# Optimization experiments

Hardware: AMD Instinct MI355X
Metric: run time of the kernel (lower is better)

The kernel has to match this reference:

```python
import jax, jax.numpy as jnp
import numpy as np

FEAT_STRIDE = 16
SCORE_THRESH = 0.7
MAX_OUTPUTS = 50


def setup_inputs() -> dict:
    key = jax.random.key(0)
    k1, k2 = jax.random.split(key)
    B = 4096
    img_width = 16384
    feat_width = img_width // FEAT_STRIDE  # 1024
    pred_cls_logit = jax.random.normal(k1, (B, feat_width), dtype=jnp.float32)
    pred_delta = jax.random.normal(k2, (B, feat_width, 2), dtype=jnp.float32)
    return {"pred_cls_logit": pred_cls_logit, "pred_delta": pred_delta, "img_width": img_width}


def _nms_single(positions, scores):
    # positions: [N,2] float32, scores: [N] float32 (post-sigmoid)
    # TF version gathers entries with score >= thresh; we keep fixed shape with a
    # validity mask (score of invalid entries set to -inf) for jit-compatibility.
    valid = scores >= SCORE_THRESH
    cent = positions.mean(axis=1)                       # [N]
    n = jnp.sum(valid).astype(jnp.float32)
    vmin = jnp.min(jnp.where(valid, cent, jnp.inf))
    vmax = jnp.max(jnp.where(valid, cent, -jnp.inf))
    # note: the original code OVERWRITES the distance_thresh arg with this value
    dthresh = 0.55 * (vmax - vmin) / (n - 1.0)
    neg_inf = jnp.float32(-jnp.inf)
    work = jnp.where(valid, scores, neg_inf)

    def step(work, _):
        idx = jnp.argmax(work)                          # greedy: highest remaining score
        ok = work[idx] > neg_inf                        # any candidate left?
        sel_s = scores[idx]
        sel_p = positions[idx]
        sel_c = cent[idx]
        # TF keeps |dist| > thresh, i.e. suppress |dist| <= thresh (incl. self)
        suppress = jnp.abs(cent - sel_c) <= dthresh
        work = jnp.where(suppress, neg_inf, work)
        out_p = jnp.where(ok, sel_p, 0.0)               # pad_to_fixed_size -> zeros
        out_s = jnp.where(ok, sel_s, 0.0)
        return work, (out_p, out_s)

    _, (nms_pos, nms_sc) = jax.lax.scan(step, work, None, length=MAX_OUTPUTS)
    return nms_pos, nms_sc[:, None]                     # [50,2], [50,1]


def reference(pred_cls_logit, pred_delta, img_width):
    feat_width = pred_delta.shape[1]
    # interval centers, broadcast over the 2-wide position pair
    centers = (jnp.arange(feat_width, dtype=jnp.float32) + 0.5) * FEAT_STRIDE  # [Fw]
    pos = pred_delta * FEAT_STRIDE + centers[None, :, None]                    # [B,Fw,2]
    w = jnp.float32(img_width)
    pos = jnp.clip(pos, 0.0, w - 1.0)
    scores = jax.nn.sigmoid(pred_cls_logit)                                    # [B,Fw]
    nms_positions, nms_scores = jax.vmap(_nms_single)(pos, scores)
    return nms_positions, nms_scores
```

## Files before the change

kernel.cpp:

```cpp
#include <hip/hip_runtime.h>
#include <stdint.h>

typedef unsigned int u32;

#define FW   1024
#define NOUT 50
#define RPB  4
#define CAP  320
#define SPL  5

#define DPP_UMAX_STEP(m, ctrl)                                                 \
  do {                                                                         \
    const u32 _t = (u32)__builtin_amdgcn_update_dpp(0, (int)(m), (ctrl),       \
                                                    0xf, 0xf, false);          \
    (m) = (m) > _t ? (m) : _t;                                                 \
  } while (0)
#define DPP_FMAX_STEP(m, ctrl)                                                 \
  do {                                                                         \
    const float _t = __uint_as_float((u32)__builtin_amdgcn_update_dpp(         \
        __float_as_int(m), __float_as_int(m), (ctrl), 0xf, 0xf, false));       \
    (m) = fmaxf((m), _t);                                                      \
  } while (0)
#define DPP_FMIN_STEP(m, ctrl)                                                 \
  do {                                                                         \
    const float _t = __uint_as_float((u32)__builtin_amdgcn_update_dpp(         \
        __float_as_int(m), __float_as_int(m), (ctrl), 0xf, 0xf, false));       \
    (m) = fminf((m), _t);                                                      \
  } while (0)
#define DPP_SCAN_STEP(x, ctrl, rmask)                                          \
  do {                                                                         \
    const int _t = __builtin_amdgcn_update_dpp(0, (x), (ctrl), (rmask), 0xf,   \
                                               false);                         \
    (x) += _t;                                                                 \
  } while (0)

#define DPP_ALL6(OP, a)                                                        \
  OP(a, 0x111); OP(a, 0x112); OP(a, 0x114); OP(a, 0x118); OP(a, 0x142);        \
  OP(a, 0x143)

__device__ __forceinline__ u32 umax2(u32 a, u32 b) { return a > b ? a : b; }
__device__ __forceinline__ u32 umax3(u32 a, u32 b, u32 c) {
  return umax2(umax2(a, b), c);
}

template <int NS>
__device__ __forceinline__ u32 run_nms(const float2* __restrict__ kc, int nc,
                                       int lane, float dthresh) {
  u32 keys[NS];
  float cents[NS];
  {
    float2 sl[NS];
#pragma unroll
    for (int k = 0; k < NS; ++k) sl[k] = kc[k * 64 + lane];
#pragma unroll
    for (int k = 0; k < NS; ++k) {
      const int q2 = k * 64 + lane;
      keys[k]  = (q2 < nc) ? __float_as_uint(sl[k].x) : 0u;
      cents[k] = sl[k].y;
    }
  }

  u32 acckey = 0;
#pragma unroll
  for (int it = 0; it < NOUT; ++it) {
    u32 m = umax3(keys[0], keys[1], keys[2]);
#pragma unroll
    for (int k = 3; k < NS; ++k) m = umax2(m, keys[k]);
    DPP_UMAX_STEP(m, 0x111);
    DPP_UMAX_STEP(m, 0x112);
    DPP_UMAX_STEP(m, 0x114);
    DPP_UMAX_STEP(m, 0x118);
    DPP_UMAX_STEP(m, 0x142);
    DPP_UMAX_STEP(m, 0x143);
    const u32 best = (u32)__builtin_amdgcn_readlane((int)m, 63);

    const int qs  = 511 - (int)(best & 511u);
    const int qsc = qs < CAP ? qs : CAP - 1;
    const float sel_c = kc[qsc].y;

    acckey = (lane == it) ? best : acckey;

#pragma unroll
    for (int k = 0; k < NS; ++k) {
      keys[k] = (fabsf(cents[k] - sel_c) <= dthresh) ? 0u : keys[k];
    }
  }
  return acckey;
}

__global__ __launch_bounds__(256, 4) void nms1d_kernel(
    const float* __restrict__ logits,
    const float* __restrict__ delta,
    const int* __restrict__ iw_p,
    float* __restrict__ out_pos,
    float* __restrict__ out_sc)
{
  const int wave = threadIdx.x >> 6;
  const int lane = threadIdx.x & 63;
  const int b = blockIdx.x * RPB + wave;

  __shared__ float2 s_kc[RPB][CAP + 1];
  __shared__ float2 s_pp[RPB][CAP + 1];
  float2* __restrict__ kc = s_kc[wave];
  float2* __restrict__ pp = s_pp[wave];

  const float hi = (float)(*iw_p) - 1.0f;

  const float* __restrict__ lrow = logits + (size_t)b * FW;
  const float* __restrict__ drow = delta  + (size_t)b * FW * 2;

  float4 xl0 = *(const float4*)(lrow + lane * 16 + 0);
  float4 xl1 = *(const float4*)(lrow + lane * 16 + 4);
  float4 xl2 = *(const float4*)(lrow + lane * 16 + 8);
  float4 xl3 = *(const float4*)(lrow + lane * 16 + 12);
  float4 dA0 = *(const float4*)(drow + lane * 32 + 0);
  float4 dB0 = *(const float4*)(drow + lane * 32 + 4);
  float4 dA1 = *(const float4*)(drow + lane * 32 + 8);
  float4 dB1 = *(const float4*)(drow + lane * 32 + 12);
  float4 dA2 = *(const float4*)(drow + lane * 32 + 16);
  float4 dB2 = *(const float4*)(drow + lane * 32 + 20);
  float4 dA3 = *(const float4*)(drow + lane * 32 + 24);
  float4 dB3 = *(const float4*)(drow + lane * 32 + 28);

  float sc[16];
  int v = 0;
  const float4 xls[4] = {xl0, xl1, xl2, xl3};
#pragma unroll
  for (int c = 0; c < 4; ++c) {
    const float xs[4] = {xls[c].x, xls[c].y, xls[c].z, xls[c].w};
#pragma unroll
    for (int j = 0; j < 4; ++j) {
      const float s = 1.0f / (1.0f + expf(-xs[j]));
      sc[c * 4 + j] = s;
      v += (s >= 0.7f) ? 1 : 0;
    }
  }

  int incl = v;
  DPP_SCAN_STEP(incl, 0x111, 0xf);
  DPP_SCAN_STEP(incl, 0x112, 0xf);
  DPP_SCAN_STEP(incl, 0x114, 0xf);
  DPP_SCAN_STEP(incl, 0x118, 0xf);
  DPP_SCAN_STEP(incl, 0x142, 0xa);
  DPP_SCAN_STEP(incl, 0x143, 0xc);
  const int base = incl - v;
  const int n = __builtin_amdgcn_readlane(incl, 63);

  float vmin = INFINITY, vmax = -INFINITY;
  int q = base;
  const float4 dAs[4] = {dA0, dA1, dA2, dA3};
  const float4 dBs[4] = {dB0, dB1, dB2, dB3};
#pragma unroll
  for (int c = 0; c < 4; ++c) {
    const float dx[4] = {dAs[c].x, dAs[c].z, dBs[c].x, dBs[c].z};
    const float dy[4] = {dAs[c].y, dAs[c].w, dBs[c].y, dBs[c].w};
#pragma unroll
    for (int j = 0; j < 4; ++j) {
      const int e = c * 4 + j;
      const int f = lane * 16 + e;
      const float center = (float)f * 16.0f + 8.0f;
      float p0 = dx[j] * 16.0f + center;
      float p1 = dy[j] * 16.0f + center;
      p0 = fminf(fmaxf(p0, 0.0f), hi);
      p1 = fminf(fmaxf(p1, 0.0f), hi);
      const float cc = (p0 + p1) * 0.5f;
      const float s = sc[e];
      const bool valid = (s >= 0.7f);
      vmin = valid ? fminf(vmin, cc) : vmin;
      vmax = valid ? fmaxf(vmax, cc) : vmax;
      const int qd = (valid && q < CAP) ? q : CAP;
      const u32 key = ((__float_as_uint(s) - 0x3F333333u) << 9) | (u32)(511 - q);
      kc[qd] = make_float2(__uint_as_float(key), cc);
      pp[qd] = make_float2(p0, p1);
      q += valid ? 1 : 0;
    }
  }

  DPP_ALL6(DPP_FMIN_STEP, vmin);
  DPP_ALL6(DPP_FMAX_STEP, vmax);
  const float dt_part = (0.55f * (vmax - vmin)) / ((float)incl - 1.0f);
  const float dthresh = __uint_as_float(
      (u32)__builtin_amdgcn_readlane(__float_as_int(dt_part), 63));

  const int nc = n < CAP ? n : CAP;
  u32 acckey;
  if (nc <= 256) acckey = run_nms<4>(kc, nc, lane, dthresh);
  else           acckey = run_nms<5>(kc, nc, lane, dthresh);

  if (lane < NOUT) {
    float p0 = 0.0f, p1 = 0.0f, s = 0.0f;
    if (acckey != 0u) {
      const int qw = 511 - (int)(acckey & 511u);
      const float2 sl = pp[qw];
      p0 = sl.x;
      p1 = sl.y;
      s  = __uint_as_float((acckey >> 9) + 0x3F333333u);
    }
    float* __restrict__ orow_p = out_pos + (size_t)b * NOUT * 2;
    float* __restrict__ orow_s = out_sc  + (size_t)b * NOUT;
    *(float2*)(orow_p + lane * 2) = make_float2(p0, p1);
    orow_s[lane] = s;
  }
}

extern "C" void kernel_launch(void* const* d_in, const int* in_sizes, int n_in,
                              void* d_out, int out_size, void* d_ws, size_t ws_size,
                              hipStream_t stream) {
  const float* logits = (const float*)d_in[0];
  const float* delta  = (const float*)d_in[1];
  const int*   iw     = (const int*)d_in[2];
  const int B = in_sizes[0] / FW;
  float* out_pos = (float*)d_out;
  float* out_sc  = (float*)d_out + (size_t)B * NOUT * 2;
  nms1d_kernel<<<(B + RPB - 1) / RPB, RPB * 64, 0, stream>>>(logits, delta, iw, out_pos, out_sc);
}
```

Measured before the change: 25.69 us.

## Process two rows per wave with interleaved NMS loops for ILP

Each wave now handles two batch rows and runs their greedy NMS loops interleaved, so the serial max-reduce, readlane and LDS-lookup chains of one row can overlap with the other's. This aims to hide the latency of the dependent per-iteration reduction. In exchange register pressure roughly doubles (launch bounds drop from 4 to 2 blocks per SM), there are half as many waves in total, and the 5-slot path runs whenever either row needs it.

```diff
diff --git a/kernel.cpp b/kernel.cpp
--- a/kernel.cpp
+++ b/kernel.cpp
@@ -5,7 +5,8 @@
 
 #define FW   1024
 #define NOUT 50
-#define RPB  4
+#define WPB  4
+#define RPW  2
 #define CAP  320
 #define SPL  5
 
@@ -44,51 +45,67 @@
 }
 
 template <int NS>
-__device__ __forceinline__ u32 run_nms(const float2* __restrict__ kc, int nc,
-                                       int lane, float dthresh) {
-  u32 keys[NS];
-  float cents[NS];
+__device__ __forceinline__ void run_nms2(
+    const float2* __restrict__ kcA, const float2* __restrict__ kcB,
+    int ncA, int ncB, int lane, float dtA, float dtB,
+    u32& accA_o, u32& accB_o)
+{
+  u32 keysA[NS], keysB[NS];
+  float centsA[NS], centsB[NS];
   {
-    float2 sl[NS];
-#pragma unroll
-    for (int k = 0; k < NS; ++k) sl[k] = kc[k * 64 + lane];
+    float2 slA[NS], slB[NS];
+#pragma unroll
+    for (int k = 0; k < NS; ++k) {
+      slA[k] = kcA[k * 64 + lane];
+      slB[k] = kcB[k * 64 + lane];
+    }
 #pragma unroll
     for (int k = 0; k < NS; ++k) {
       const int q2 = k * 64 + lane;
-      keys[k]  = (q2 < nc) ? __float_as_uint(sl[k].x) : 0u;
-      cents[k] = sl[k].y;
-    }
-  }
-
-  u32 acckey = 0;
-#pragma unroll
+      keysA[k]  = (q2 < ncA) ? __float_as_uint(slA[k].x) : 0u;
+      keysB[k]  = (q2 < ncB) ? __float_as_uint(slB[k].x) : 0u;
+      centsA[k] = slA[k].y;
+      centsB[k] = slB[k].y;
+    }
+  }
+
+  u32 accA = 0, accB = 0;
+#pragma unroll 2
   for (int it = 0; it < NOUT; ++it) {
-    u32 m = umax3(keys[0], keys[1], keys[2]);
-#pragma unroll
-    for (int k = 3; k < NS; ++k) m = umax2(m, keys[k]);
-    DPP_UMAX_STEP(m, 0x111);
-    DPP_UMAX_STEP(m, 0x112);
-    DPP_UMAX_STEP(m, 0x114);
-    DPP_UMAX_STEP(m, 0x118);
-    DPP_UMAX_STEP(m, 0x142);
-    DPP_UMAX_STEP(m, 0x143);
-    const u32 best = (u32)__builtin_amdgcn_readlane((int)m, 63);
-
-    const int qs  = 511 - (int)(best & 511u);
-    const int qsc = qs < CAP ? qs : CAP - 1;
-    const float sel_c = kc[qsc].y;
-
-    acckey = (lane == it) ? best : acckey;
+    u32 mA = umax3(keysA[0], keysA[1], keysA[2]);
+    u32 mB = umax3(keysB[0], keysB[1], keysB[2]);
+#pragma unroll
+    for (int k = 3; k < NS; ++k) { mA = umax2(mA, keysA[k]); mB = umax2(mB, keysB[k]); }
+    DPP_UMAX_STEP(mA, 0x111); DPP_UMAX_STEP(mB, 0x111);
+    DPP_UMAX_STEP(mA, 0x112); DPP_UMAX_STEP(mB, 0x112);
+    DPP_UMAX_STEP(mA, 0x114); DPP_UMAX_STEP(mB, 0x114);
+    DPP_UMAX_STEP(mA, 0x118); DPP_UMAX_STEP(mB, 0x118);
+    DPP_UMAX_STEP(mA, 0x142); DPP_UMAX_STEP(mB, 0x142);
+    DPP_UMAX_STEP(mA, 0x143); DPP_UMAX_STEP(mB, 0x143);
+    const u32 bestA = (u32)__builtin_amdgcn_readlane((int)mA, 63);
+    const u32 bestB = (u32)__builtin_amdgcn_readlane((int)mB, 63);
+
+    const int qsA  = 511 - (int)(bestA & 511u);
+    const int qsB  = 511 - (int)(bestB & 511u);
+    const int qscA = qsA < CAP ? qsA : CAP - 1;
+    const int qscB = qsB < CAP ? qsB : CAP - 1;
+    const float selA = kcA[qscA].y;
+    const float selB = kcB[qscB].y;
+
+    accA = (lane == it) ? bestA : accA;
+    accB = (lane == it) ? bestB : accB;
 
 #pragma unroll
     for (int k = 0; k < NS; ++k) {
-      keys[k] = (fabsf(cents[k] - sel_c) <= dthresh) ? 0u : keys[k];
-    }
-  }
-  return acckey;
-}
-
-__global__ __launch_bounds__(256, 4) void nms1d_kernel(
+      keysA[k] = (fabsf(centsA[k] - selA) <= dtA) ? 0u : keysA[k];
+      keysB[k] = (fabsf(centsB[k] - selB) <= dtB) ? 0u : keysB[k];
+    }
+  }
+  accA_o = accA;
+  accB_o = accB;
+}
+
+__global__ __launch_bounds__(256, 2) void nms1d_kernel(
     const float* __restrict__ logits,
     const float* __restrict__ delta,
     const int* __restrict__ iw_p,
@@ -97,109 +114,126 @@
 {
   const int wave = threadIdx.x >> 6;
   const int lane = threadIdx.x & 63;
-  const int b = blockIdx.x * RPB + wave;
-
-  __shared__ float2 s_kc[RPB][CAP + 1];
-  __shared__ float2 s_pp[RPB][CAP + 1];
-  float2* __restrict__ kc = s_kc[wave];
-  float2* __restrict__ pp = s_pp[wave];
+  const int b0 = (blockIdx.x * WPB + wave) * RPW;
+
+  __shared__ float2 s_kc[WPB][RPW][CAP + 1];
+  __shared__ float2 s_pp[WPB][RPW][CAP + 1];
 
   const float hi = (float)(*iw_p) - 1.0f;
 
-  const float* __restrict__ lrow = logits + (size_t)b * FW;
-  const float* __restrict__ drow = delta  + (size_t)b * FW * 2;
-
-  float4 xl0 = *(const float4*)(lrow + lane * 16 + 0);
-  float4 xl1 = *(const float4*)(lrow + lane * 16 + 4);
-  float4 xl2 = *(const float4*)(lrow + lane * 16 + 8);
-  float4 xl3 = *(const float4*)(lrow + lane * 16 + 12);
-  float4 dA0 = *(const float4*)(drow + lane * 32 + 0);
-  float4 dB0 = *(const float4*)(drow + lane * 32 + 4);
-  float4 dA1 = *(const float4*)(drow + lane * 32 + 8);
-  float4 dB1 = *(const float4*)(drow + lane * 32 + 12);
-  float4 dA2 = *(const float4*)(drow + lane * 32 + 16);
-  float4 dB2 = *(const float4*)(drow + lane * 32 + 20);
-  float4 dA3 = *(const float4*)(drow + lane * 32 + 24);
-  float4 dB3 = *(const float4*)(drow + lane * 32 + 28);
-
-  float sc[16];
-  int v = 0;
-  const float4 xls[4] = {xl0, xl1, xl2, xl3};
-#pragma unroll
-  for (int c = 0; c < 4; ++c) {
-    const float xs[4] = {xls[c].x, xls[c].y, xls[c].z, xls[c].w};
-#pragma unroll
-    for (int j = 0; j < 4; ++j) {
-      const float s = 1.0f / (1.0f + expf(-xs[j]));
-      sc[c * 4 + j] = s;
-      v += (s >= 0.7f) ? 1 : 0;
-    }
-  }
-
-  int incl = v;
-  DPP_SCAN_STEP(incl, 0x111, 0xf);
-  DPP_SCAN_STEP(incl, 0x112, 0xf);
-  DPP_SCAN_STEP(incl, 0x114, 0xf);
-  DPP_SCAN_STEP(incl, 0x118, 0xf);
-  DPP_SCAN_STEP(incl, 0x142, 0xa);
-  DPP_SCAN_STEP(incl, 0x143, 0xc);
-  const int base = incl - v;
-  const int n = __builtin_amdgcn_readlane(incl, 63);
-
-  float vmin = INFINITY, vmax = -INFINITY;
-  int q = base;
-  const float4 dAs[4] = {dA0, dA1, dA2, dA3};
-  const float4 dBs[4] = {dB0, dB1, dB2, dB3};
-#pragma unroll
-  for (int c = 0; c < 4; ++c) {
-    const float dx[4] = {dAs[c].x, dAs[c].z, dBs[c].x, dBs[c].z};
-    const float dy[4] = {dAs[c].y, dAs[c].w, dBs[c].y, dBs[c].w};
-#pragma unroll
-    for (int j = 0; j < 4; ++j) {
-      const int e = c * 4 + j;
-      const int f = lane * 16 + e;
-      const float center = (float)f * 16.0f + 8.0f;
-      float p0 = dx[j] * 16.0f + center;
-      float p1 = dy[j] * 16.0f + center;
-      p0 = fminf(fmaxf(p0, 0.0f), hi);
-      p1 = fminf(fmaxf(p1, 0.0f), hi);
-      const float cc = (p0 + p1) * 0.5f;
-      const float s = sc[e];
-      const bool valid = (s >= 0.7f);
-      vmin = valid ? fminf(vmin, cc) : vmin;
-      vmax = valid ? fmaxf(vmax, cc) : vmax;
-      const int qd = (valid && q < CAP) ? q : CAP;
-      const u32 key = ((__float_as_uint(s) - 0x3F333333u) << 9) | (u32)(511 - q);
-      kc[qd] = make_float2(__uint_as_float(key), cc);
-      pp[qd] = make_float2(p0, p1);
-      q += valid ? 1 : 0;
-    }
-  }
-
-  DPP_ALL6(DPP_FMIN_STEP, vmin);
-  DPP_ALL6(DPP_FMAX_STEP, vmax);
-  const float dt_part = (0.55f * (vmax - vmin)) / ((float)incl - 1.0f);
-  const float dthresh = __uint_as_float(
-      (u32)__builtin_amdgcn_readlane(__float_as_int(dt_part), 63));
-
-  const int nc = n < CAP ? n : CAP;
-  u32 acckey;
-  if (nc <= 256) acckey = run_nms<4>(kc, nc, lane, dthresh);
-  else           acckey = run_nms<5>(kc, nc, lane, dthresh);
+  float4 xl[RPW][4], dXa[RPW][4], dXb[RPW][4];
+#pragma unroll
+  for (int r = 0; r < RPW; ++r) {
+    const float* __restrict__ lrow = logits + (size_t)(b0 + r) * FW;
+#pragma unroll
+    for (int c = 0; c < 4; ++c)
+      xl[r][c] = *(const float4*)(lrow + lane * 16 + 4 * c);
+  }
+#pragma unroll
+  for (int r = 0; r < RPW; ++r) {
+    const float* __restrict__ drow = delta + (size_t)(b0 + r) * FW * 2;
+#pragma unroll
+    for (int c = 0; c < 4; ++c) {
+      dXa[r][c] = *(const float4*)(drow + lane * 32 + 8 * c);
+      dXb[r][c] = *(const float4*)(drow + lane * 32 + 8 * c + 4);
+    }
+  }
+
+  float sc[RPW][16];
+  int incl[RPW], base_[RPW];
+#pragma unroll
+  for (int r = 0; r < RPW; ++r) {
+    int v = 0;
+#pragma unroll
+    for (int c = 0; c < 4; ++c) {
+      const float xs[4] = {xl[r][c].x, xl[r][c].y, xl[r][c].z, xl[r][c].w};
+#pragma unroll
+      for (int j = 0; j < 4; ++j) {
+        const float s = 1.0f / (1.0f + expf(-xs[j]));
+        sc[r][c * 4 + j] = s;
+        v += (s >= 0.7f) ? 1 : 0;
+      }
+    }
+    int ic = v;
+    DPP_SCAN_STEP(ic, 0x111, 0xf);
+    DPP_SCAN_STEP(ic, 0x112, 0xf);
+    DPP_SCAN_STEP(ic, 0x114, 0xf);
+    DPP_SCAN_STEP(ic, 0x118, 0xf);
+    DPP_SCAN_STEP(ic, 0x142, 0xa);
+    DPP_SCAN_STEP(ic, 0x143, 0xc);
+    incl[r]  = ic;
+    base_[r] = ic - v;
+  }
+
+  float dthr[RPW];
+  int nfin[RPW];
+#pragma unroll
+  for (int r = 0; r < RPW; ++r) {
+    float2* __restrict__ kc = s_kc[wave][r];
+    float2* __restrict__ pp = s_pp[wave][r];
+    float vmin = INFINITY, vmax = -INFINITY;
+    int q = base_[r];
+#pragma unroll
+    for (int c = 0; c < 4; ++c) {
+      const float dx[4] = {dXa[r][c].x, dXa[r][c].z, dXb[r][c].x, dXb[r][c].z};
+      const float dy[4] = {dXa[r][c].y, dXa[r][c].w, dXb[r][c].y, dXb[r][c].w};
+#pragma unroll
+      for (int j = 0; j < 4; ++j) {
+        const int e = c * 4 + j;
+        const int f = lane * 16 + e;
+        const float center = (float)f * 16.0f + 8.0f;
+        float p0 = dx[j] * 16.0f + center;
+        float p1 = dy[j] * 16.0f + center;
+        p0 = fminf(fmaxf(p0, 0.0f), hi);
+        p1 = fminf(fmaxf(p1, 0.0f), hi);
+        const float cc = (p0 + p1) * 0.5f;
+        const float s = sc[r][e];
+        const bool valid = (s >= 0.7f);
+        vmin = valid ? fminf(vmin, cc) : vmin;
+        vmax = valid ? fmaxf(vmax, cc) : vmax;
+        const int qd = (valid && q < CAP) ? q : CAP;
+        const u32 key = ((__float_as_uint(s) - 0x3F333333u) << 9) | (u32)(511 - q);
+        kc[qd] = make_float2(__uint_as_float(key), cc);
+        pp[qd] = make_float2(p0, p1);
+        q += valid ? 1 : 0;
+      }
+    }
+    DPP_ALL6(DPP_FMIN_STEP, vmin);
+    DPP_ALL6(DPP_FMAX_STEP, vmax);
+    const float dt_part = (0.55f * (vmax - vmin)) / ((float)incl[r] - 1.0f);
+    dthr[r] = __uint_as_float(
+        (u32)__builtin_amdgcn_readlane(__float_as_int(dt_part), 63));
+    nfin[r] = __builtin_amdgcn_readlane(incl[r], 63);
+  }
+
+  const int ncA = nfin[0] < CAP ? nfin[0] : CAP;
+  const int ncB = nfin[1] < CAP ? nfin[1] : CAP;
+  u32 accA, accB;
+  if (ncA <= 256 && ncB <= 256)
+    run_nms2<4>(s_kc[wave][0], s_kc[wave][1], ncA, ncB, lane,
+                dthr[0], dthr[1], accA, accB);
+  else
+    run_nms2<5>(s_kc[wave][0], s_kc[wave][1], ncA, ncB, lane,
+                dthr[0], dthr[1], accA, accB);
 
   if (lane < NOUT) {
-    float p0 = 0.0f, p1 = 0.0f, s = 0.0f;
-    if (acckey != 0u) {
-      const int qw = 511 - (int)(acckey & 511u);
-      const float2 sl = pp[qw];
-      p0 = sl.x;
-      p1 = sl.y;
-      s  = __uint_as_float((acckey >> 9) + 0x3F333333u);
-    }
-    float* __restrict__ orow_p = out_pos + (size_t)b * NOUT * 2;
-    float* __restrict__ orow_s = out_sc  + (size_t)b * NOUT;
-    *(float2*)(orow_p + lane * 2) = make_float2(p0, p1);
-    orow_s[lane] = s;
+#pragma unroll
+    for (int r = 0; r < RPW; ++r) {
+      const u32 ak = (r == 0) ? accA : accB;
+      const float2* __restrict__ pp = s_pp[wave][r];
+      float p0 = 0.0f, p1 = 0.0f, s = 0.0f;
+      if (ak != 0u) {
+        const int qw = 511 - (int)(ak & 511u);
+        const float2 sl = pp[qw];
+        p0 = sl.x;
+        p1 = sl.y;
+        s  = __uint_as_float((ak >> 9) + 0x3F333333u);
+      }
+      float* __restrict__ orow_p = out_pos + (size_t)(b0 + r) * NOUT * 2;
+      float* __restrict__ orow_s = out_sc  + (size_t)(b0 + r) * NOUT;
+      *(float2*)(orow_p + lane * 2) = make_float2(p0, p1);
+      orow_s[lane] = s;
+    }
   }
 }
 
@@ -212,5 +246,7 @@
   const int B = in_sizes[0] / FW;
   float* out_pos = (float*)d_out;
   float* out_sc  = (float*)d_out + (size_t)B * NOUT * 2;
-  nms1d_kernel<<<(B + RPB - 1) / RPB, RPB * 64, 0, stream>>>(logits, delta, iw, out_pos, out_sc);
-}
+  const int rows_per_block = WPB * RPW;
+  nms1d_kernel<<<(B + rows_per_block - 1) / rows_per_block, WPB * 64, 0, stream>>>(
+      logits, delta, iw, out_pos, out_sc);
+}
```

Result: slower. 27.28 us (+6.2%).

## Select top-two candidates per NMS iteration to halve serial greedy steps

Applied to the files above, without the earlier changes.

Each NMS iteration now runs a wave-wide top-2 reduction (max and second max via DPP) instead of only the max. If the runner-up is not suppressed by the winner, both are accepted in one pass, so the serial loop of 50 argmax rounds can take fewer rounds. The cost is a roughly doubled reduction and suppression per iteration, plus a loop that is no longer fully unrolled and runs a data-dependent number of times. The second-max tracking in the DPP step must be exactly right for results to stay correct.

```diff
diff --git a/kernel.cpp b/kernel.cpp
--- a/kernel.cpp
+++ b/kernel.cpp
@@ -15,6 +15,16 @@
                                                     0xf, 0xf, false);          \
     (m) = (m) > _t ? (m) : _t;                                                 \
   } while (0)
+#define DPP_UMAX2_STEP(m1, m2, ctrl)                                           \
+  do {                                                                         \
+    const u32 _t1 = (u32)__builtin_amdgcn_update_dpp(0, (int)(m1), (ctrl),     \
+                                                     0xf, 0xf, false);         \
+    const u32 _t2 = (u32)__builtin_amdgcn_update_dpp(0, (int)(m2), (ctrl),     \
+                                                     0xf, 0xf, false);         \
+    const u32 _c = (m1) < _t1 ? (m1) : _t1;              \
+    (m1) = (m1) > _t1 ? (m1) : _t1;                                            \
+    (m2) = umax3((m2), _t2, _c);                                               \
+  } while (0)
 #define DPP_FMAX_STEP(m, ctrl)                                                 \
   do {                                                                         \
     const float _t = __uint_as_float((u32)__builtin_amdgcn_update_dpp(         \
@@ -39,6 +49,7 @@
   OP(a, 0x143)
 
 __device__ __forceinline__ u32 umax2(u32 a, u32 b) { return a > b ? a : b; }
+__device__ __forceinline__ u32 umin2(u32 a, u32 b) { return a < b ? a : b; }
 __device__ __forceinline__ u32 umax3(u32 a, u32 b, u32 c) {
   return umax2(umax2(a, b), c);
 }
@@ -60,30 +71,47 @@
     }
   }
 
+  const float dnan = __uint_as_float(0x7FC00000u);
   u32 acckey = 0;
-#pragma unroll
-  for (int it = 0; it < NOUT; ++it) {
-    u32 m = umax3(keys[0], keys[1], keys[2]);
-#pragma unroll
-    for (int k = 3; k < NS; ++k) m = umax2(m, keys[k]);
-    DPP_UMAX_STEP(m, 0x111);
-    DPP_UMAX_STEP(m, 0x112);
-    DPP_UMAX_STEP(m, 0x114);
-    DPP_UMAX_STEP(m, 0x118);
-    DPP_UMAX_STEP(m, 0x142);
-    DPP_UMAX_STEP(m, 0x143);
-    const u32 best = (u32)__builtin_amdgcn_readlane((int)m, 63);
-
-    const int qs  = 511 - (int)(best & 511u);
-    const int qsc = qs < CAP ? qs : CAP - 1;
-    const float sel_c = kc[qsc].y;
-
-    acckey = (lane == it) ? best : acckey;
+  int it = 0;
+  while (it < NOUT) {
+    u32 m1 = umax2(keys[0], keys[1]);
+    u32 m2 = umin2(keys[0], keys[1]);
+#pragma unroll
+    for (int k = 2; k < NS; ++k) {
+      const u32 t = umin2(m1, keys[k]);
+      m1 = umax2(m1, keys[k]);
+      m2 = umax2(m2, t);
+    }
+    DPP_UMAX2_STEP(m1, m2, 0x111);
+    DPP_UMAX2_STEP(m1, m2, 0x112);
+    DPP_UMAX2_STEP(m1, m2, 0x114);
+    DPP_UMAX2_STEP(m1, m2, 0x118);
+    DPP_UMAX2_STEP(m1, m2, 0x142);
+    DPP_UMAX2_STEP(m1, m2, 0x143);
+    const u32 best1 = (u32)__builtin_amdgcn_readlane((int)m1, 63);
+    const u32 best2 = (u32)__builtin_amdgcn_readlane((int)m2, 63);
+
+    const int qs1  = 511 - (int)(best1 & 511u);
+    const int qs2  = 511 - (int)(best2 & 511u);
+    const int qsc1 = qs1 < CAP ? qs1 : CAP - 1;
+    const int qsc2 = qs2 < CAP ? qs2 : CAP - 1;
+    const float c1 = kc[qsc1].y;
+    const float c2 = kc[qsc2].y;
+
+    const bool acc2 = fabsf(c2 - c1) > dthresh;
+    const float dt2 = acc2 ? dthresh : dnan;
+
+    acckey = (lane == it) ? best1 : acckey;
+    acckey = (acc2 && lane == it + 1) ? best2 : acckey;
 
 #pragma unroll
     for (int k = 0; k < NS; ++k) {
-      keys[k] = (fabsf(cents[k] - sel_c) <= dthresh) ? 0u : keys[k];
-    }
+      keys[k] = (fabsf(cents[k] - c1) <= dthresh) ? 0u : keys[k];
+      keys[k] = (fabsf(cents[k] - c2) <= dt2)     ? 0u : keys[k];
+    }
+
+    it += __builtin_amdgcn_readfirstlane(acc2 ? 2 : 1);
   }
   return acckey;
 }
```

Result: slower. 27.95 us (+8.8%).

## Process two rows per wave, prefetching second row during first row's NMS

Applied to the files above, without the earlier changes.

Each wave now handles two batch rows. The global loads for the second row are issued before the first row's greedy NMS loop, so memory latency overlaps with compute. The grid is halved and launch bounds drop to 2 blocks per CU, which allows more registers for the prefetched data but may reduce occupancy and latency hiding across waves. There is also a risk that the compiler serializes the second row's loads or that the prefetched row spills registers.

```diff
diff --git a/kernel.cpp b/kernel.cpp
--- a/kernel.cpp
+++ b/kernel.cpp
@@ -5,7 +5,8 @@
 
 #define FW   1024
 #define NOUT 50
-#define RPB  4
+#define WPB  4
+#define RPW  2
 #define CAP  320
 #define SPL  5
 
@@ -43,91 +44,35 @@
   return umax2(umax2(a, b), c);
 }
 
-template <int NS>
-__device__ __forceinline__ u32 run_nms(const float2* __restrict__ kc, int nc,
-                                       int lane, float dthresh) {
-  u32 keys[NS];
-  float cents[NS];
-  {
-    float2 sl[NS];
-#pragma unroll
-    for (int k = 0; k < NS; ++k) sl[k] = kc[k * 64 + lane];
-#pragma unroll
-    for (int k = 0; k < NS; ++k) {
-      const int q2 = k * 64 + lane;
-      keys[k]  = (q2 < nc) ? __float_as_uint(sl[k].x) : 0u;
-      cents[k] = sl[k].y;
-    }
-  }
-
-  u32 acckey = 0;
-#pragma unroll
-  for (int it = 0; it < NOUT; ++it) {
-    u32 m = umax3(keys[0], keys[1], keys[2]);
-#pragma unroll
-    for (int k = 3; k < NS; ++k) m = umax2(m, keys[k]);
-    DPP_UMAX_STEP(m, 0x111);
-    DPP_UMAX_STEP(m, 0x112);
-    DPP_UMAX_STEP(m, 0x114);
-    DPP_UMAX_STEP(m, 0x118);
-    DPP_UMAX_STEP(m, 0x142);
-    DPP_UMAX_STEP(m, 0x143);
-    const u32 best = (u32)__builtin_amdgcn_readlane((int)m, 63);
-
-    const int qs  = 511 - (int)(best & 511u);
-    const int qsc = qs < CAP ? qs : CAP - 1;
-    const float sel_c = kc[qsc].y;
-
-    acckey = (lane == it) ? best : acckey;
-
-#pragma unroll
-    for (int k = 0; k < NS; ++k) {
-      keys[k] = (fabsf(cents[k] - sel_c) <= dthresh) ? 0u : keys[k];
-    }
-  }
-  return acckey;
-}
-
-__global__ __launch_bounds__(256, 4) void nms1d_kernel(
-    const float* __restrict__ logits,
-    const float* __restrict__ delta,
-    const int* __restrict__ iw_p,
-    float* __restrict__ out_pos,
-    float* __restrict__ out_sc)
-{
-  const int wave = threadIdx.x >> 6;
-  const int lane = threadIdx.x & 63;
-  const int b = blockIdx.x * RPB + wave;
-
-  __shared__ float2 s_kc[RPB][CAP + 1];
-  __shared__ float2 s_pp[RPB][CAP + 1];
-  float2* __restrict__ kc = s_kc[wave];
-  float2* __restrict__ pp = s_pp[wave];
-
-  const float hi = (float)(*iw_p) - 1.0f;
-
+struct RowData {
+  float4 xl[4];
+  float4 da[4];
+  float4 db[4];
+};
+
+__device__ __forceinline__ void load_row(const float* __restrict__ logits,
+                                         const float* __restrict__ delta,
+                                         int b, int lane, RowData& d) {
   const float* __restrict__ lrow = logits + (size_t)b * FW;
   const float* __restrict__ drow = delta  + (size_t)b * FW * 2;
-
-  float4 xl0 = *(const float4*)(lrow + lane * 16 + 0);
-  float4 xl1 = *(const float4*)(lrow + lane * 16 + 4);
-  float4 xl2 = *(const float4*)(lrow + lane * 16 + 8);
-  float4 xl3 = *(const float4*)(lrow + lane * 16 + 12);
-  float4 dA0 = *(const float4*)(drow + lane * 32 + 0);
-  float4 dB0 = *(const float4*)(drow + lane * 32 + 4);
-  float4 dA1 = *(const float4*)(drow + lane * 32 + 8);
-  float4 dB1 = *(const float4*)(drow + lane * 32 + 12);
-  float4 dA2 = *(const float4*)(drow + lane * 32 + 16);
-  float4 dB2 = *(const float4*)(drow + lane * 32 + 20);
-  float4 dA3 = *(const float4*)(drow + lane * 32 + 24);
-  float4 dB3 = *(const float4*)(drow + lane * 32 + 28);
-
+#pragma unroll
+  for (int c = 0; c < 4; ++c)
+    d.xl[c] = *(const float4*)(lrow + lane * 16 + 4 * c);
+#pragma unroll
+  for (int c = 0; c < 4; ++c) {
+    d.da[c] = *(const float4*)(drow + lane * 32 + 8 * c);
+    d.db[c] = *(const float4*)(drow + lane * 32 + 8 * c + 4);
+  }
+}
+
+__device__ __forceinline__ void prep_row(const RowData& d, float2* __restrict__ kc,
+                                         float2* __restrict__ pp, int lane,
+                                         float hi, float& dthresh_o, int& nc_o) {
   float sc[16];
   int v = 0;
-  const float4 xls[4] = {xl0, xl1, xl2, xl3};
 #pragma unroll
   for (int c = 0; c < 4; ++c) {
-    const float xs[4] = {xls[c].x, xls[c].y, xls[c].z, xls[c].w};
+    const float xs[4] = {d.xl[c].x, d.xl[c].y, d.xl[c].z, d.xl[c].w};
 #pragma unroll
     for (int j = 0; j < 4; ++j) {
       const float s = 1.0f / (1.0f + expf(-xs[j]));
@@ -148,12 +93,10 @@
 
   float vmin = INFINITY, vmax = -INFINITY;
   int q = base;
-  const float4 dAs[4] = {dA0, dA1, dA2, dA3};
-  const float4 dBs[4] = {dB0, dB1, dB2, dB3};
 #pragma unroll
   for (int c = 0; c < 4; ++c) {
-    const float dx[4] = {dAs[c].x, dAs[c].z, dBs[c].x, dBs[c].z};
-    const float dy[4] = {dAs[c].y, dAs[c].w, dBs[c].y, dBs[c].w};
+    const float dx[4] = {d.da[c].x, d.da[c].z, d.db[c].x, d.db[c].z};
+    const float dy[4] = {d.da[c].y, d.da[c].w, d.db[c].y, d.db[c].w};
 #pragma unroll
     for (int j = 0; j < 4; ++j) {
       const int e = c * 4 + j;
@@ -179,14 +122,60 @@
   DPP_ALL6(DPP_FMIN_STEP, vmin);
   DPP_ALL6(DPP_FMAX_STEP, vmax);
   const float dt_part = (0.55f * (vmax - vmin)) / ((float)incl - 1.0f);
-  const float dthresh = __uint_as_float(
+  dthresh_o = __uint_as_float(
       (u32)__builtin_amdgcn_readlane(__float_as_int(dt_part), 63));
-
-  const int nc = n < CAP ? n : CAP;
-  u32 acckey;
-  if (nc <= 256) acckey = run_nms<4>(kc, nc, lane, dthresh);
-  else           acckey = run_nms<5>(kc, nc, lane, dthresh);
-
+  nc_o = n < CAP ? n : CAP;
+}
+
+template <int NS>
+__device__ __forceinline__ u32 run_nms(const float2* __restrict__ kc, int nc,
+                                       int lane, float dthresh) {
+  u32 keys[NS];
+  float cents[NS];
+  {
+    float2 sl[NS];
+#pragma unroll
+    for (int k = 0; k < NS; ++k) sl[k] = kc[k * 64 + lane];
+#pragma unroll
+    for (int k = 0; k < NS; ++k) {
+      const int q2 = k * 64 + lane;
+      keys[k]  = (q2 < nc) ? __float_as_uint(sl[k].x) : 0u;
+      cents[k] = sl[k].y;
+    }
+  }
+
+  u32 acckey = 0;
+#pragma unroll
+  for (int it = 0; it < NOUT; ++it) {
+    u32 m = umax3(keys[0], keys[1], keys[2]);
+#pragma unroll
+    for (int k = 3; k < NS; ++k) m = umax2(m, keys[k]);
+    DPP_UMAX_STEP(m, 0x111);
+    DPP_UMAX_STEP(m, 0x112);
+    DPP_UMAX_STEP(m, 0x114);
+    DPP_UMAX_STEP(m, 0x118);
+    DPP_UMAX_STEP(m, 0x142);
+    DPP_UMAX_STEP(m, 0x143);
+    const u32 best = (u32)__builtin_amdgcn_readlane((int)m, 63);
+
+    const int qs  = 511 - (int)(best & 511u);
+    const int qsc = qs < CAP ? qs : CAP - 1;
+    const float sel_c = kc[qsc].y;
+
+    acckey = (lane == it) ? best : acckey;
+
+#pragma unroll
+    for (int k = 0; k < NS; ++k) {
+      keys[k] = (fabsf(cents[k] - sel_c) <= dthresh) ? 0u : keys[k];
+    }
+  }
+  return acckey;
+}
+
+__device__ __forceinline__ void epilogue_row(const float2* __restrict__ pp,
+                                             u32 acckey, int b, int lane,
+                                             float* __restrict__ out_pos,
+                                             float* __restrict__ out_sc) {
   if (lane < NOUT) {
     float p0 = 0.0f, p1 = 0.0f, s = 0.0f;
     if (acckey != 0u) {
@@ -201,6 +190,45 @@
     *(float2*)(orow_p + lane * 2) = make_float2(p0, p1);
     orow_s[lane] = s;
   }
+}
+
+__global__ __launch_bounds__(256, 2) void nms1d_kernel(
+    const float* __restrict__ logits,
+    const float* __restrict__ delta,
+    const int* __restrict__ iw_p,
+    float* __restrict__ out_pos,
+    float* __restrict__ out_sc)
+{
+  const int wave = threadIdx.x >> 6;
+  const int lane = threadIdx.x & 63;
+  const int b0 = (blockIdx.x * WPB + wave) * RPW;
+
+  __shared__ float2 s_kc[WPB][CAP + 1];
+  __shared__ float2 s_pp[WPB][CAP + 1];
+  float2* __restrict__ kc = s_kc[wave];
+  float2* __restrict__ pp = s_pp[wave];
+
+  const float hi = (float)(*iw_p) - 1.0f;
+
+  RowData A;
+  load_row(logits, delta, b0, lane, A);
+  float dtA; int ncA;
+  prep_row(A, kc, pp, lane, hi, dtA, ncA);
+
+  RowData Bv;
+  load_row(logits, delta, b0 + 1, lane, Bv);
+
+  u32 accA;
+  if (ncA <= 256) accA = run_nms<4>(kc, ncA, lane, dtA);
+  else            accA = run_nms<5>(kc, ncA, lane, dtA);
+  epilogue_row(pp, accA, b0, lane, out_pos, out_sc);
+
+  float dtB; int ncB;
+  prep_row(Bv, kc, pp, lane, hi, dtB, ncB);
+  u32 accB;
+  if (ncB <= 256) accB = run_nms<4>(kc, ncB, lane, dtB);
+  else            accB = run_nms<5>(kc, ncB, lane, dtB);
+  epilogue_row(pp, accB, b0 + 1, lane, out_pos, out_sc);
 }
 
 extern "C" void kernel_launch(void* const* d_in, const int* in_sizes, int n_in,
@@ -212,5 +240,7 @@
   const int B = in_sizes[0] / FW;
   float* out_pos = (float*)d_out;
   float* out_sc  = (float*)d_out + (size_t)B * NOUT * 2;
-  nms1d_kernel<<<(B + RPB - 1) / RPB, RPB * 64, 0, stream>>>(logits, delta, iw, out_pos, out_sc);
-}
+  const int rows_per_block = WPB * RPW;
+  nms1d_kernel<<<(B + rows_per_block - 1) / rows_per_block, WPB * 64, 0, stream>>>(
+      logits, delta, iw, out_pos, out_sc);
+}
```

Measured after the change: 29.65 us. +15.4%, slower.
